# Kernel tuning notes

Measured on AMD Instinct MI355X. Metric: run time of the kernel, lower is better.

Reference implementation:

```python
import jax, jax.numpy as jnp
import numpy as np

N_BATCH, C, H, W = 4, 64, 64, 64


def setup_inputs() -> dict:
    key = jax.random.key(0)
    ks = jax.random.split(key, 8)
    x = jax.random.normal(ks[0], (N_BATCH, C, H, W), dtype=jnp.float32)
    wb = jax.random.normal(ks[1], (C, C), dtype=jnp.float32) * 0.05
    bb = jax.random.normal(ks[2], (C,), dtype=jnp.float32) * 0.05
    wc = jax.random.normal(ks[3], (C, C), dtype=jnp.float32) * 0.05
    bc = jax.random.normal(ks[4], (C,), dtype=jnp.float32) * 0.05
    wd = jax.random.normal(ks[5], (C, C), dtype=jnp.float32) * 0.05
    bd = jax.random.normal(ks[6], (C,), dtype=jnp.float32) * 0.05
    alpha = jax.random.normal(ks[7], (1,), dtype=jnp.float32)
    return {"x": x, "wb": wb, "bb": bb, "wc": wc, "bc": bc,
            "wd": wd, "bd": bd, "alpha": alpha}


def reference(x, wb, bb, wc, bc, wd, bd, alpha):
    n, c, h, w = x.shape
    xf = x.reshape(n, c, h * w)  # (n, c, L)
    # 1x1 convs == per-pixel channel GEMMs
    xb = jnp.einsum('oc,ncl->nol', wb, xf) + bb[None, :, None]  # keys   (n, c, L)
    xc = jnp.einsum('oc,ncl->nol', wc, xf) + bc[None, :, None]  # queries(n, c, L)
    xd = jnp.einsum('oc,ncl->nol', wd, xf) + bd[None, :, None]  # values (n, c, L)
    # attention[i, j] = <xc[:, i], xb[:, j]>, softmax over j
    attention = jnp.einsum('nci,ncj->nij', xc, xb)  # (n, L, L)
    att = jax.nn.softmax(attention, axis=-1)
    # x_o[:, :, i] = sum_j xd[:, :, j] * att[i, j]
    x_o = jnp.einsum('ncj,nij->nci', xd, att).reshape(n, c, h, w)
    return alpha[0] * x_o + x
```

## Files before the change

kernel.cpp:

```cpp
#include <hip/hip_runtime.h>
#include <hip/hip_bf16.h>

typedef unsigned short u16;
typedef unsigned char u8;
typedef unsigned int u32;
typedef long long i64;
typedef __attribute__((ext_vector_type(4))) float f32x4;
typedef __attribute__((ext_vector_type(4))) unsigned int u32x4;

#define L_SEQ 4096
#define NCH 64
#define NBATCH 4
#define NW 8
#define KVSPAN (L_SEQ / NW)
#define TPS (KVSPAN / 64)
#define QB 32
#define LOG2E 1.4426950408889634f
#define C2 (3.0f * LOG2E)

template <bool WORD>
__device__ inline u32 pk_fp8(float a, float b, u32 old) {
    return (u32)__builtin_amdgcn_cvt_pk_fp8_f32(a, b, (int)old, WORD);
}
__device__ inline u8 fp8_1(float a) {
    return (u8)(__builtin_amdgcn_cvt_pk_fp8_f32(a, a, 0, false) & 0xff);
}

union F8 { u32 u[2]; i64 ll; };

__global__ __launch_bounds__(256) void qkv_kernel(
    const float* __restrict__ x,
    const float* __restrict__ wb, const float* __restrict__ bb,
    const float* __restrict__ wc, const float* __restrict__ bc,
    const float* __restrict__ wd, const float* __restrict__ bd,
    u8* __restrict__ Qp8, u8* __restrict__ Kp8, u8* __restrict__ Vp8)
{
    __shared__ float xs[64][64];
    __shared__ float wl[3][64][65];

    const int nb  = blockIdx.y;
    const int i0  = blockIdx.x * 64;
    const int tid = threadIdx.x;

    const float* xbase = x + (size_t)nb * NCH * L_SEQ + i0;
    #pragma unroll
    for (int rep = 0; rep < 16; ++rep) {
        int idx = rep * 256 + tid;
        int c = idx >> 6, px = idx & 63;
        xs[c][px] = xbase[(size_t)c * L_SEQ + px];
    }
    const float* wsrc[3] = { wb, wc, wd };
    for (int m = 0; m < 3; ++m) {
        #pragma unroll
        for (int rep = 0; rep < 16; ++rep) {
            int idx = rep * 256 + tid;
            wl[m][idx >> 6][idx & 63] = wsrc[m][idx];
        }
    }
    __syncthreads();

    const int co  = tid & 63;
    const int pg  = tid >> 6;
    const int px0 = pg * 16;

    float accB[16], accC[16], accD[16];
    const float biasB = bb[co], biasC = bc[co], biasD = bd[co];
    #pragma unroll
    for (int p = 0; p < 16; ++p) { accB[p] = biasB; accC[p] = biasC; accD[p] = biasD; }

    for (int c = 0; c < 64; ++c) {
        const float wbv = wl[0][co][c];
        const float wcv = wl[1][co][c];
        const float wdv = wl[2][co][c];
        #pragma unroll
        for (int p = 0; p < 16; ++p) {
            const float xv = xs[c][px0 + p];
            accB[p] += wbv * xv;
            accC[p] += wcv * xv;
            accD[p] += wdv * xv;
        }
    }

    const size_t nbase = (size_t)nb * L_SEQ * NCH;
    const int jb     = i0 / 16 + pg;
    const int kbase8 = ((co & 31) >> 3) * 256 + (co >> 5) * 8 + (co & 7);
    const int vbase8 = (i0 >> 6) * 4096 + (co >> 4) * 1024 + (co & 15) * 16
                     + (pg >> 1) * 8 + (pg & 1) * 4;

    #pragma unroll
    for (int p = 0; p < 16; ++p) {
        const int i = i0 + px0 + p;
        Kp8[nbase + jb * 1024 + kbase8 + p * 16] = fp8_1(accB[p]);
        Qp8[nbase + (size_t)i * 64 + co]         = fp8_1(accC[p] * LOG2E);
    }
    #pragma unroll
    for (int pq = 0; pq < 4; ++pq) {
        u32 wv = pk_fp8<false>(accD[pq * 4 + 0], accD[pq * 4 + 1], 0);
        wv     = pk_fp8<true >(accD[pq * 4 + 2], accD[pq * 4 + 3], wv);
        *(u32*)&Vp8[nbase + vbase8 + pq * 256] = wv;
    }
}

__global__ __launch_bounds__(512, 4) void attn_kernel(
    const u8* __restrict__ Qp8, const u8* __restrict__ Kp8,
    const u8* __restrict__ Vp8, const float* __restrict__ x,
    const float* __restrict__ alphap, float* __restrict__ out)
{
    __shared__ float smem[NW][QB * 65];
    __shared__ float lbuf[NW][QB];

    const int nb   = blockIdx.y;
    const int i0   = blockIdx.x * QB;
    const int tid  = threadIdx.x;
    const int w    = tid >> 6;
    const int lane = tid & 63;
    const int lo   = lane & 15;
    const int hi   = lane >> 4;

    i64 qf[2][2];
    #pragma unroll
    for (int qt = 0; qt < 2; ++qt) {
        const u8* qrow = Qp8 + (size_t)(nb * L_SEQ + i0 + qt * 16 + lo) * 64;
        qf[qt][0] = *(const i64*)(qrow + hi * 8);
        qf[qt][1] = *(const i64*)(qrow + 32 + hi * 8);
    }

    const f32x4 zero = { 0.f, 0.f, 0.f, 0.f };
    f32x4 acc_o[2][4];
    #pragma unroll
    for (int qt = 0; qt < 2; ++qt)
        #pragma unroll
        for (int ct = 0; ct < 4; ++ct) acc_o[qt][ct] = zero;
    float l_[2] = { 0.f, 0.f };

    const u8* KpB = Kp8 + (size_t)nb * L_SEQ * NCH;
    const u8* VpB = Vp8 + (size_t)nb * NCH * L_SEQ;

    #pragma unroll 1
    for (int t = 0; t < TPS; ++t) {
        const int j0 = w * KVSPAN + t * 64;

        u32x4 kw[4], vw[4];
        #pragma unroll
        for (int jt = 0; jt < 4; ++jt)
            kw[jt] = *(const u32x4*)(KpB + (size_t)(j0 / 16 + jt) * 1024 + lane * 16);
        #pragma unroll
        for (int ct = 0; ct < 4; ++ct)
            vw[ct] = *(const u32x4*)(VpB + (size_t)(j0 >> 6) * 4096 + ct * 1024 + lane * 16);

        f32x4 s[2][4];
        #pragma unroll
        for (int jt = 0; jt < 4; ++jt) {
            F8 k0, k1;
            k0.u[0] = kw[jt][0]; k0.u[1] = kw[jt][1];
            k1.u[0] = kw[jt][2]; k1.u[1] = kw[jt][3];
            #pragma unroll
            for (int qt = 0; qt < 2; ++qt) {
                f32x4 a = zero;
                a = __builtin_amdgcn_mfma_f32_16x16x32_fp8_fp8(k0.ll, qf[qt][0], a, 0, 0, 0);
                a = __builtin_amdgcn_mfma_f32_16x16x32_fp8_fp8(k1.ll, qf[qt][1], a, 0, 0, 0);
                s[qt][jt] = a;
            }
        }

        F8 pf[2][2];
        #pragma unroll
        for (int qt = 0; qt < 2; ++qt) {
            #pragma unroll
            for (int jt = 0; jt < 4; ++jt)
                #pragma unroll
                for (int r = 0; r < 4; ++r)
                    s[qt][jt][r] = exp2f(s[qt][jt][r] - C2);

            const float t0 = (s[qt][0][0] + s[qt][0][1]) + (s[qt][0][2] + s[qt][0][3]);
            const float t1 = (s[qt][1][0] + s[qt][1][1]) + (s[qt][1][2] + s[qt][1][3]);
            const float t2 = (s[qt][2][0] + s[qt][2][1]) + (s[qt][2][2] + s[qt][2][3]);
            const float t3 = (s[qt][3][0] + s[qt][3][1]) + (s[qt][3][2] + s[qt][3][3]);
            float rs = (t0 + t1) + (t2 + t3);
            rs += __shfl_xor(rs, 16, 64);
            rs += __shfl_xor(rs, 32, 64);
            l_[qt] += rs;

            pf[qt][0].u[0] = pk_fp8<true>(s[qt][0][2], s[qt][0][3], pk_fp8<false>(s[qt][0][0], s[qt][0][1], 0));
            pf[qt][0].u[1] = pk_fp8<true>(s[qt][1][2], s[qt][1][3], pk_fp8<false>(s[qt][1][0], s[qt][1][1], 0));
            pf[qt][1].u[0] = pk_fp8<true>(s[qt][2][2], s[qt][2][3], pk_fp8<false>(s[qt][2][0], s[qt][2][1], 0));
            pf[qt][1].u[1] = pk_fp8<true>(s[qt][3][2], s[qt][3][3], pk_fp8<false>(s[qt][3][0], s[qt][3][1], 0));
        }

        #pragma unroll
        for (int ct = 0; ct < 4; ++ct) {
            F8 v0, v1;
            v0.u[0] = vw[ct][0]; v0.u[1] = vw[ct][1];
            v1.u[0] = vw[ct][2]; v1.u[1] = vw[ct][3];
            #pragma unroll
            for (int qt = 0; qt < 2; ++qt) {
                acc_o[qt][ct] = __builtin_amdgcn_mfma_f32_16x16x32_fp8_fp8(v0.ll, pf[qt][0].ll, acc_o[qt][ct], 0, 0, 0);
                acc_o[qt][ct] = __builtin_amdgcn_mfma_f32_16x16x32_fp8_fp8(v1.ll, pf[qt][1].ll, acc_o[qt][ct], 0, 0, 0);
            }
        }
    }

    #pragma unroll
    for (int qt = 0; qt < 2; ++qt)
        #pragma unroll
        for (int ct = 0; ct < 4; ++ct)
            #pragma unroll
            for (int r = 0; r < 4; ++r)
                smem[w][(qt * 16 + lo) * 65 + ct * 16 + hi * 4 + r] = acc_o[qt][ct][r];
    if (hi == 0) {
        lbuf[w][lo]      = l_[0];
        lbuf[w][16 + lo] = l_[1];
    }
    __syncthreads();

    const int q  = tid & 31;
    const int c0 = (tid >> 5) * 4;

    float Ls = 0.f, O[4] = { 0.f, 0.f, 0.f, 0.f };
    #pragma unroll
    for (int s2 = 0; s2 < NW; ++s2) {
        Ls += lbuf[s2][q];
        #pragma unroll
        for (int k = 0; k < 4; ++k)
            O[k] += smem[s2][q * 65 + c0 + k];
    }
    const float rl    = __builtin_amdgcn_rcpf(Ls);
    const float alpha = alphap[0];

    #pragma unroll
    for (int k = 0; k < 4; ++k) {
        const size_t idx = ((size_t)(nb * NCH + c0 + k)) * L_SEQ + i0 + q;
        out[idx] = alpha * O[k] * rl + x[idx];
    }
}

extern "C" void kernel_launch(void* const* d_in, const int* in_sizes, int n_in,
                              void* d_out, int out_size, void* d_ws, size_t ws_size,
                              hipStream_t stream) {
    const float* x     = (const float*)d_in[0];
    const float* wb    = (const float*)d_in[1];
    const float* bb    = (const float*)d_in[2];
    const float* wc    = (const float*)d_in[3];
    const float* bc    = (const float*)d_in[4];
    const float* wd    = (const float*)d_in[5];
    const float* bd    = (const float*)d_in[6];
    const float* alpha = (const float*)d_in[7];

    const size_t elems = (size_t)NBATCH * L_SEQ * NCH;
    u8* Qp8 = (u8*)d_ws;
    u8* Kp8 = Qp8 + elems;
    u8* Vp8 = Kp8 + elems;

    qkv_kernel<<<dim3(L_SEQ / 64, NBATCH), 256, 0, stream>>>(
        x, wb, bb, wc, bc, wd, bd, Qp8, Kp8, Vp8);
    attn_kernel<<<dim3(L_SEQ / QB, NBATCH), 512, 0, stream>>>(
        Qp8, Kp8, Vp8, x, alpha, (float*)d_out);
}
```

Measured before the change: 42.96 us.

## Double query block per workgroup and stage partial outputs in bf16 shared memory

```diff
diff --git a/kernel.cpp b/kernel.cpp
--- a/kernel.cpp
+++ b/kernel.cpp
@@ -7,6 +7,7 @@
 typedef long long i64;
 typedef __attribute__((ext_vector_type(4))) float f32x4;
 typedef __attribute__((ext_vector_type(4))) unsigned int u32x4;
+typedef __attribute__((ext_vector_type(2))) unsigned int uint2_t;
 
 #define L_SEQ 4096
 #define NCH 64
@@ -14,7 +15,8 @@
 #define NW 8
 #define KVSPAN (L_SEQ / NW)
 #define TPS (KVSPAN / 64)
-#define QB 32
+#define QB 64
+#define SMS 72
 #define LOG2E 1.4426950408889634f
 #define C2 (3.0f * LOG2E)
 
@@ -24,6 +26,11 @@
 }
 __device__ inline u8 fp8_1(float a) {
     return (u8)(__builtin_amdgcn_cvt_pk_fp8_f32(a, a, 0, false) & 0xff);
+}
+__device__ inline u32 cvtpk_bf(float a, float b) {
+    u32 r;
+    asm("v_cvt_pk_bf16_f32 %0, %1, %2" : "=v"(r) : "v"(a), "v"(b));
+    return r;
 }
 
 union F8 { u32 u[2]; i64 ll; };
@@ -101,12 +108,12 @@
     }
 }
 
-__global__ __launch_bounds__(512, 4) void attn_kernel(
+__global__ __launch_bounds__(512, 2) void attn_kernel(
     const u8* __restrict__ Qp8, const u8* __restrict__ Kp8,
     const u8* __restrict__ Vp8, const float* __restrict__ x,
     const float* __restrict__ alphap, float* __restrict__ out)
 {
-    __shared__ float smem[NW][QB * 65];
+    __shared__ u16 smem[NW][QB * SMS];
     __shared__ float lbuf[NW][QB];
 
     const int nb   = blockIdx.y;
@@ -117,21 +124,21 @@
     const int lo   = lane & 15;
     const int hi   = lane >> 4;
 
-    i64 qf[2][2];
-    #pragma unroll
-    for (int qt = 0; qt < 2; ++qt) {
+    i64 qf[4][2];
+    #pragma unroll
+    for (int qt = 0; qt < 4; ++qt) {
         const u8* qrow = Qp8 + (size_t)(nb * L_SEQ + i0 + qt * 16 + lo) * 64;
         qf[qt][0] = *(const i64*)(qrow + hi * 8);
         qf[qt][1] = *(const i64*)(qrow + 32 + hi * 8);
     }
 
     const f32x4 zero = { 0.f, 0.f, 0.f, 0.f };
-    f32x4 acc_o[2][4];
-    #pragma unroll
-    for (int qt = 0; qt < 2; ++qt)
+    f32x4 acc_o[4][4];
+    #pragma unroll
+    for (int qt = 0; qt < 4; ++qt)
         #pragma unroll
         for (int ct = 0; ct < 4; ++ct) acc_o[qt][ct] = zero;
-    float l_[2] = { 0.f, 0.f };
+    float l_[4] = { 0.f, 0.f, 0.f, 0.f };
 
     const u8* KpB = Kp8 + (size_t)nb * L_SEQ * NCH;
     const u8* VpB = Vp8 + (size_t)nb * NCH * L_SEQ;
@@ -148,87 +155,89 @@
         for (int ct = 0; ct < 4; ++ct)
             vw[ct] = *(const u32x4*)(VpB + (size_t)(j0 >> 6) * 4096 + ct * 1024 + lane * 16);
 
-        f32x4 s[2][4];
-        #pragma unroll
-        for (int jt = 0; jt < 4; ++jt) {
-            F8 k0, k1;
-            k0.u[0] = kw[jt][0]; k0.u[1] = kw[jt][1];
-            k1.u[0] = kw[jt][2]; k1.u[1] = kw[jt][3];
+        #pragma unroll
+        for (int qt = 0; qt < 4; ++qt) {
+            f32x4 s[4];
             #pragma unroll
-            for (int qt = 0; qt < 2; ++qt) {
+            for (int jt = 0; jt < 4; ++jt) {
+                F8 k0, k1;
+                k0.u[0] = kw[jt][0]; k0.u[1] = kw[jt][1];
+                k1.u[0] = kw[jt][2]; k1.u[1] = kw[jt][3];
                 f32x4 a = zero;
                 a = __builtin_amdgcn_mfma_f32_16x16x32_fp8_fp8(k0.ll, qf[qt][0], a, 0, 0, 0);
                 a = __builtin_amdgcn_mfma_f32_16x16x32_fp8_fp8(k1.ll, qf[qt][1], a, 0, 0, 0);
-                s[qt][jt] = a;
+                s[jt] = a;
             }
-        }
-
-        F8 pf[2][2];
-        #pragma unroll
-        for (int qt = 0; qt < 2; ++qt) {
+
             #pragma unroll
             for (int jt = 0; jt < 4; ++jt)
                 #pragma unroll
                 for (int r = 0; r < 4; ++r)
-                    s[qt][jt][r] = exp2f(s[qt][jt][r] - C2);
-
-            const float t0 = (s[qt][0][0] + s[qt][0][1]) + (s[qt][0][2] + s[qt][0][3]);
-            const float t1 = (s[qt][1][0] + s[qt][1][1]) + (s[qt][1][2] + s[qt][1][3]);
-            const float t2 = (s[qt][2][0] + s[qt][2][1]) + (s[qt][2][2] + s[qt][2][3]);
-            const float t3 = (s[qt][3][0] + s[qt][3][1]) + (s[qt][3][2] + s[qt][3][3]);
+                    s[jt][r] = exp2f(s[jt][r] - C2);
+
+            const float t0 = (s[0][0] + s[0][1]) + (s[0][2] + s[0][3]);
+            const float t1 = (s[1][0] + s[1][1]) + (s[1][2] + s[1][3]);
+            const float t2 = (s[2][0] + s[2][1]) + (s[2][2] + s[2][3]);
+            const float t3 = (s[3][0] + s[3][1]) + (s[3][2] + s[3][3]);
             float rs = (t0 + t1) + (t2 + t3);
             rs += __shfl_xor(rs, 16, 64);
             rs += __shfl_xor(rs, 32, 64);
             l_[qt] += rs;
 
-            pf[qt][0].u[0] = pk_fp8<true>(s[qt][0][2], s[qt][0][3], pk_fp8<false>(s[qt][0][0], s[qt][0][1], 0));
-            pf[qt][0].u[1] = pk_fp8<true>(s[qt][1][2], s[qt][1][3], pk_fp8<false>(s[qt][1][0], s[qt][1][1], 0));
-            pf[qt][1].u[0] = pk_fp8<true>(s[qt][2][2], s[qt][2][3], pk_fp8<false>(s[qt][2][0], s[qt][2][1], 0));
-            pf[qt][1].u[1] = pk_fp8<true>(s[qt][3][2], s[qt][3][3], pk_fp8<false>(s[qt][3][0], s[qt][3][1], 0));
-        }
-
+            F8 pf0, pf1;
+            pf0.u[0] = pk_fp8<true>(s[0][2], s[0][3], pk_fp8<false>(s[0][0], s[0][1], 0));
+            pf0.u[1] = pk_fp8<true>(s[1][2], s[1][3], pk_fp8<false>(s[1][0], s[1][1], 0));
+            pf1.u[0] = pk_fp8<true>(s[2][2], s[2][3], pk_fp8<false>(s[2][0], s[2][1], 0));
+            pf1.u[1] = pk_fp8<true>(s[3][2], s[3][3], pk_fp8<false>(s[3][0], s[3][1], 0));
+
+            #pragma unroll
+            for (int ct = 0; ct < 4; ++ct) {
+                F8 v0, v1;
+                v0.u[0] = vw[ct][0]; v0.u[1] = vw[ct][1];
+                v1.u[0] = vw[ct][2]; v1.u[1] = vw[ct][3];
+                acc_o[qt][ct] = __builtin_amdgcn_mfma_f32_16x16x32_fp8_fp8(v0.ll, pf0.ll, acc_o[qt][ct], 0, 0, 0);
+                acc_o[qt][ct] = __builtin_amdgcn_mfma_f32_16x16x32_fp8_fp8(v1.ll, pf1.ll, acc_o[qt][ct], 0, 0, 0);
+            }
+        }
+    }
+
+    #pragma unroll
+    for (int qt = 0; qt < 4; ++qt) {
         #pragma unroll
         for (int ct = 0; ct < 4; ++ct) {
-            F8 v0, v1;
-            v0.u[0] = vw[ct][0]; v0.u[1] = vw[ct][1];
-            v1.u[0] = vw[ct][2]; v1.u[1] = vw[ct][3];
-            #pragma unroll
-            for (int qt = 0; qt < 2; ++qt) {
-                acc_o[qt][ct] = __builtin_amdgcn_mfma_f32_16x16x32_fp8_fp8(v0.ll, pf[qt][0].ll, acc_o[qt][ct], 0, 0, 0);
-                acc_o[qt][ct] = __builtin_amdgcn_mfma_f32_16x16x32_fp8_fp8(v1.ll, pf[qt][1].ll, acc_o[qt][ct], 0, 0, 0);
-            }
-        }
-    }
-
-    #pragma unroll
-    for (int qt = 0; qt < 2; ++qt)
-        #pragma unroll
-        for (int ct = 0; ct < 4; ++ct)
-            #pragma unroll
-            for (int r = 0; r < 4; ++r)
-                smem[w][(qt * 16 + lo) * 65 + ct * 16 + hi * 4 + r] = acc_o[qt][ct][r];
-    if (hi == 0) {
-        lbuf[w][lo]      = l_[0];
-        lbuf[w][16 + lo] = l_[1];
+            uint2_t pk;
+            pk[0] = cvtpk_bf(acc_o[qt][ct][0], acc_o[qt][ct][1]);
+            pk[1] = cvtpk_bf(acc_o[qt][ct][2], acc_o[qt][ct][3]);
+            *(uint2_t*)&smem[w][(qt * 16 + lo) * SMS + ct * 16 + hi * 4] = pk;
+        }
+        if (hi == 0) lbuf[w][qt * 16 + lo] = l_[qt];
     }
     __syncthreads();
 
-    const int q  = tid & 31;
-    const int c0 = (tid >> 5) * 4;
-
-    float Ls = 0.f, O[4] = { 0.f, 0.f, 0.f, 0.f };
+    const int q  = tid & 63;
+    const int c0 = (tid >> 6) * 8;
+
+    float Ls = 0.f, O[8];
+    #pragma unroll
+    for (int k = 0; k < 8; ++k) O[k] = 0.f;
     #pragma unroll
     for (int s2 = 0; s2 < NW; ++s2) {
         Ls += lbuf[s2][q];
-        #pragma unroll
-        for (int k = 0; k < 4; ++k)
-            O[k] += smem[s2][q * 65 + c0 + k];
+        const u32x4 pv = *(const u32x4*)&smem[s2][q * SMS + c0];
+        #pragma unroll
+        for (int k2 = 0; k2 < 4; ++k2) {
+            union { u32 u; float f; } a, b;
+            a.u = (pv[k2] & 0xffffu) << 16;
+            b.u = pv[k2] & 0xffff0000u;
+            O[k2 * 2]     += a.f;
+            O[k2 * 2 + 1] += b.f;
+        }
     }
     const float rl    = __builtin_amdgcn_rcpf(Ls);
     const float alpha = alphap[0];
 
     #pragma unroll
-    for (int k = 0; k < 4; ++k) {
+    for (int k = 0; k < 8; ++k) {
         const size_t idx = ((size_t)(nb * NCH + c0 + k)) * L_SEQ + i0 + q;
         out[idx] = alpha * O[k] * rl + x[idx];
     }
```

Result: no change. 42.82 us (-0.3%).

## Switch attention MFMAs to 32x32x64 scaled FP8 with matching K/V layouts

Applied to the files above, without the earlier changes.

```diff
diff --git a/kernel.cpp b/kernel.cpp
--- a/kernel.cpp
+++ b/kernel.cpp
@@ -4,9 +4,9 @@
 typedef unsigned short u16;
 typedef unsigned char u8;
 typedef unsigned int u32;
-typedef long long i64;
-typedef __attribute__((ext_vector_type(4))) float f32x4;
 typedef __attribute__((ext_vector_type(4))) unsigned int u32x4;
+typedef __attribute__((ext_vector_type(8))) int i32x8;
+typedef __attribute__((ext_vector_type(16))) float f32x16;
 
 #define L_SEQ 4096
 #define NCH 64
@@ -17,6 +17,7 @@
 #define QB 32
 #define LOG2E 1.4426950408889634f
 #define C2 (3.0f * LOG2E)
+#define SCL1 127
 
 template <bool WORD>
 __device__ inline u32 pk_fp8(float a, float b, u32 old) {
@@ -26,7 +27,8 @@
     return (u8)(__builtin_amdgcn_cvt_pk_fp8_f32(a, a, 0, false) & 0xff);
 }
 
-union F8 { u32 u[2]; i64 ll; };
+union I8 { u32x4 q[2]; i32x8 v; };
+union PU { u32 u[8]; i32x8 v; };
 
 __global__ __launch_bounds__(256) void qkv_kernel(
     const float* __restrict__ x,
@@ -82,22 +84,23 @@
     }
 
     const size_t nbase = (size_t)nb * L_SEQ * NCH;
-    const int jb     = i0 / 16 + pg;
-    const int kbase8 = ((co & 31) >> 3) * 256 + (co >> 5) * 8 + (co & 7);
-    const int vbase8 = (i0 >> 6) * 4096 + (co >> 4) * 1024 + (co & 15) * 16
-                     + (pg >> 1) * 8 + (pg & 1) * 4;
+
+    const int kbase2 = (i0 >> 5) * 2048 + (pg >> 1) * 2048 + ((co >> 4) & 1) * 1024
+                     + (co >> 5) * 512 + (pg & 1) * 256 + (co & 15);
+    const int vbase2 = (i0 >> 6) * 4096 + (co >> 5) * 2048 + (pg >> 1) * 1024
+                     + (co & 31) * 16 + (pg & 1) * 8;
 
     #pragma unroll
     for (int p = 0; p < 16; ++p) {
         const int i = i0 + px0 + p;
-        Kp8[nbase + jb * 1024 + kbase8 + p * 16] = fp8_1(accB[p]);
-        Qp8[nbase + (size_t)i * 64 + co]         = fp8_1(accC[p] * LOG2E);
-    }
-    #pragma unroll
-    for (int pq = 0; pq < 4; ++pq) {
-        u32 wv = pk_fp8<false>(accD[pq * 4 + 0], accD[pq * 4 + 1], 0);
-        wv     = pk_fp8<true >(accD[pq * 4 + 2], accD[pq * 4 + 3], wv);
-        *(u32*)&Vp8[nbase + vbase8 + pq * 256] = wv;
+        Kp8[nbase + kbase2 + p * 16]     = fp8_1(accB[p]);
+        Qp8[nbase + (size_t)i * 64 + co] = fp8_1(accC[p] * LOG2E);
+    }
+    #pragma unroll
+    for (int k = 0; k < 4; ++k) {
+        u32 wv = pk_fp8<false>(accD[k * 4 + 0], accD[k * 4 + 1], 0);
+        wv     = pk_fp8<true >(accD[k * 4 + 2], accD[k * 4 + 3], wv);
+        *(u32*)&Vp8[nbase + vbase2 + (k & 1) * 512 + (k >> 1) * 4] = wv;
     }
 }
 
@@ -114,24 +117,18 @@
     const int tid  = threadIdx.x;
     const int w    = tid >> 6;
     const int lane = tid & 63;
-    const int lo   = lane & 15;
-    const int hi   = lane >> 4;
-
-    i64 qf[2][2];
-    #pragma unroll
-    for (int qt = 0; qt < 2; ++qt) {
-        const u8* qrow = Qp8 + (size_t)(nb * L_SEQ + i0 + qt * 16 + lo) * 64;
-        qf[qt][0] = *(const i64*)(qrow + hi * 8);
-        qf[qt][1] = *(const i64*)(qrow + 32 + hi * 8);
-    }
-
-    const f32x4 zero = { 0.f, 0.f, 0.f, 0.f };
-    f32x4 acc_o[2][4];
-    #pragma unroll
-    for (int qt = 0; qt < 2; ++qt)
-        #pragma unroll
-        for (int ct = 0; ct < 4; ++ct) acc_o[qt][ct] = zero;
-    float l_[2] = { 0.f, 0.f };
+    const int i_l  = lane & 31;
+    const int h2   = lane >> 5;
+
+    I8 qf;
+    {
+        const u8* qrow = Qp8 + (size_t)(nb * L_SEQ + i0 + i_l) * 64 + h2 * 32;
+        qf.q[0] = *(const u32x4*)(qrow);
+        qf.q[1] = *(const u32x4*)(qrow + 16);
+    }
+
+    f32x16 acc[2] = {};
+    float l_ = 0.f;
 
     const u8* KpB = Kp8 + (size_t)nb * L_SEQ * NCH;
     const u8* VpB = Vp8 + (size_t)nb * NCH * L_SEQ;
@@ -140,77 +137,69 @@
     for (int t = 0; t < TPS; ++t) {
         const int j0 = w * KVSPAN + t * 64;
 
-        u32x4 kw[4], vw[4];
-        #pragma unroll
-        for (int jt = 0; jt < 4; ++jt)
-            kw[jt] = *(const u32x4*)(KpB + (size_t)(j0 / 16 + jt) * 1024 + lane * 16);
-        #pragma unroll
-        for (int ct = 0; ct < 4; ++ct)
-            vw[ct] = *(const u32x4*)(VpB + (size_t)(j0 >> 6) * 4096 + ct * 1024 + lane * 16);
-
-        f32x4 s[2][4];
-        #pragma unroll
-        for (int jt = 0; jt < 4; ++jt) {
-            F8 k0, k1;
-            k0.u[0] = kw[jt][0]; k0.u[1] = kw[jt][1];
-            k1.u[0] = kw[jt][2]; k1.u[1] = kw[jt][3];
-            #pragma unroll
-            for (int qt = 0; qt < 2; ++qt) {
-                f32x4 a = zero;
-                a = __builtin_amdgcn_mfma_f32_16x16x32_fp8_fp8(k0.ll, qf[qt][0], a, 0, 0, 0);
-                a = __builtin_amdgcn_mfma_f32_16x16x32_fp8_fp8(k1.ll, qf[qt][1], a, 0, 0, 0);
-                s[qt][jt] = a;
-            }
-        }
-
-        F8 pf[2][2];
-        #pragma unroll
-        for (int qt = 0; qt < 2; ++qt) {
-            #pragma unroll
-            for (int jt = 0; jt < 4; ++jt)
-                #pragma unroll
-                for (int r = 0; r < 4; ++r)
-                    s[qt][jt][r] = exp2f(s[qt][jt][r] - C2);
-
-            const float t0 = (s[qt][0][0] + s[qt][0][1]) + (s[qt][0][2] + s[qt][0][3]);
-            const float t1 = (s[qt][1][0] + s[qt][1][1]) + (s[qt][1][2] + s[qt][1][3]);
-            const float t2 = (s[qt][2][0] + s[qt][2][1]) + (s[qt][2][2] + s[qt][2][3]);
-            const float t3 = (s[qt][3][0] + s[qt][3][1]) + (s[qt][3][2] + s[qt][3][3]);
-            float rs = (t0 + t1) + (t2 + t3);
-            rs += __shfl_xor(rs, 16, 64);
+        I8 kf0, kf1, vf0, vf1;
+        {
+            const u8* kb = KpB + (size_t)(j0 >> 5) * 2048 + lane * 16;
+            kf0.q[0] = *(const u32x4*)(kb);
+            kf0.q[1] = *(const u32x4*)(kb + 1024);
+            kf1.q[0] = *(const u32x4*)(kb + 2048);
+            kf1.q[1] = *(const u32x4*)(kb + 3072);
+            const u8* vb = VpB + (size_t)(j0 >> 6) * 4096 + lane * 16;
+            vf0.q[0] = *(const u32x4*)(vb);
+            vf0.q[1] = *(const u32x4*)(vb + 1024);
+            vf1.q[0] = *(const u32x4*)(vb + 2048);
+            vf1.q[1] = *(const u32x4*)(vb + 3072);
+        }
+
+        f32x16 z = {};
+        f32x16 s0 = __builtin_amdgcn_mfma_scale_f32_32x32x64_f8f6f4(
+            kf0.v, qf.v, z, 0, 0, 0, SCL1, 0, SCL1);
+        f32x16 s1 = __builtin_amdgcn_mfma_scale_f32_32x32x64_f8f6f4(
+            kf1.v, qf.v, z, 0, 0, 0, SCL1, 0, SCL1);
+
+        #pragma unroll
+        for (int r = 0; r < 16; ++r) {
+            s0[r] = exp2f(s0[r] - C2);
+            s1[r] = exp2f(s1[r] - C2);
+        }
+        {
+            const float a0 = (s0[0] + s0[1]) + (s0[2] + s0[3]);
+            const float a1 = (s0[4] + s0[5]) + (s0[6] + s0[7]);
+            const float a2 = (s0[8] + s0[9]) + (s0[10] + s0[11]);
+            const float a3 = (s0[12] + s0[13]) + (s0[14] + s0[15]);
+            const float b0 = (s1[0] + s1[1]) + (s1[2] + s1[3]);
+            const float b1 = (s1[4] + s1[5]) + (s1[6] + s1[7]);
+            const float b2 = (s1[8] + s1[9]) + (s1[10] + s1[11]);
+            const float b3 = (s1[12] + s1[13]) + (s1[14] + s1[15]);
+            float rs = ((a0 + a1) + (a2 + a3)) + ((b0 + b1) + (b2 + b3));
             rs += __shfl_xor(rs, 32, 64);
-            l_[qt] += rs;
-
-            pf[qt][0].u[0] = pk_fp8<true>(s[qt][0][2], s[qt][0][3], pk_fp8<false>(s[qt][0][0], s[qt][0][1], 0));
-            pf[qt][0].u[1] = pk_fp8<true>(s[qt][1][2], s[qt][1][3], pk_fp8<false>(s[qt][1][0], s[qt][1][1], 0));
-            pf[qt][1].u[0] = pk_fp8<true>(s[qt][2][2], s[qt][2][3], pk_fp8<false>(s[qt][2][0], s[qt][2][1], 0));
-            pf[qt][1].u[1] = pk_fp8<true>(s[qt][3][2], s[qt][3][3], pk_fp8<false>(s[qt][3][0], s[qt][3][1], 0));
-        }
-
-        #pragma unroll
-        for (int ct = 0; ct < 4; ++ct) {
-            F8 v0, v1;
-            v0.u[0] = vw[ct][0]; v0.u[1] = vw[ct][1];
-            v1.u[0] = vw[ct][2]; v1.u[1] = vw[ct][3];
-            #pragma unroll
-            for (int qt = 0; qt < 2; ++qt) {
-                acc_o[qt][ct] = __builtin_amdgcn_mfma_f32_16x16x32_fp8_fp8(v0.ll, pf[qt][0].ll, acc_o[qt][ct], 0, 0, 0);
-                acc_o[qt][ct] = __builtin_amdgcn_mfma_f32_16x16x32_fp8_fp8(v1.ll, pf[qt][1].ll, acc_o[qt][ct], 0, 0, 0);
-            }
-        }
-    }
-
-    #pragma unroll
-    for (int qt = 0; qt < 2; ++qt)
-        #pragma unroll
-        for (int ct = 0; ct < 4; ++ct)
-            #pragma unroll
-            for (int r = 0; r < 4; ++r)
-                smem[w][(qt * 16 + lo) * 65 + ct * 16 + hi * 4 + r] = acc_o[qt][ct][r];
-    if (hi == 0) {
-        lbuf[w][lo]      = l_[0];
-        lbuf[w][16 + lo] = l_[1];
-    }
+            l_ += rs;
+        }
+
+        PU pb;
+        #pragma unroll
+        for (int r = 0; r < 4; ++r)
+            pb.u[r] = pk_fp8<true>(s0[4 * r + 2], s0[4 * r + 3],
+                      pk_fp8<false>(s0[4 * r], s0[4 * r + 1], 0));
+        #pragma unroll
+        for (int r = 0; r < 4; ++r)
+            pb.u[4 + r] = pk_fp8<true>(s1[4 * r + 2], s1[4 * r + 3],
+                          pk_fp8<false>(s1[4 * r], s1[4 * r + 1], 0));
+
+        acc[0] = __builtin_amdgcn_mfma_scale_f32_32x32x64_f8f6f4(
+            vf0.v, pb.v, acc[0], 0, 0, 0, SCL1, 0, SCL1);
+        acc[1] = __builtin_amdgcn_mfma_scale_f32_32x32x64_f8f6f4(
+            vf1.v, pb.v, acc[1], 0, 0, 0, SCL1, 0, SCL1);
+    }
+
+    #pragma unroll
+    for (int ct = 0; ct < 2; ++ct)
+        #pragma unroll
+        for (int r = 0; r < 16; ++r) {
+            const int c = ct * 32 + (r & 3) + 8 * (r >> 2) + 4 * h2;
+            smem[w][i_l * 65 + c] = acc[ct][r];
+        }
+    if (h2 == 0) lbuf[w][i_l] = l_;
     __syncthreads();
 
     const int q  = tid & 31;
```

Result: faster. 40.83 us (-4.9%).
